# Performance work log

Measured on AMD Instinct MI355X. Metric: run time of the kernel, lower is better.

Reference implementation:

```python
import jax, jax.numpy as jnp
import numpy as np

B, C_IN, N, WIDTH, MODES, OUT_CH, DEG = 4, 3, 8192, 128, 32, 1, 16
NT = B * N


def _gelu(v):
    return jax.nn.gelu(v, approximate=False)  # torch nn.GELU default = exact erf


def _seg_mean(msg, dst, n):
    # PyG aggr='mean': zero-degree nodes get 0
    s = jax.ops.segment_sum(msg, dst, num_segments=n)
    c = jax.ops.segment_sum(jnp.ones((dst.shape[0], 1), msg.dtype), dst, num_segments=n)
    return s / jnp.maximum(c, 1.0)


def _inorm(v, eps=1e-5):
    # nn.InstanceNorm1d(width): per (batch, channel) over length, no affine
    m = v.mean(-1, keepdims=True)
    var = v.var(-1, keepdims=True)
    return (v - m) / jnp.sqrt(var + eps)


def _fourier(v, wr, wi):
    n = v.shape[-1]
    vf = jnp.fft.rfft(v, axis=-1)  # [B, width, n//2+1] complex64
    w = wr + 1j * wi               # [width, width, modes]
    of = jnp.einsum('bix,iox->box', vf[:, :, :MODES], w)
    of = jnp.pad(of, ((0, 0), (0, 0), (0, n // 2 + 1 - MODES)))
    return jnp.fft.irfft(of, n=n, axis=-1)


def _conv1(v, w, b):
    # Conv1d kernel_size=1 == channel-mixing GEMM
    return jnp.einsum('bin,oi->bon', v, w) + b[None, :, None]


def setup_inputs() -> dict:
    key = jax.random.key(0)
    ks = jax.random.split(key, 24)
    x = jax.random.normal(ks[0], (B, C_IN, N), jnp.float32)
    # edges: per-graph random neighbors + self loops (radius_graph(loop=True) surrogate)
    dst = jnp.repeat(jnp.arange(NT), DEG)
    gid = dst // N
    src = jax.random.randint(ks[1], (NT * DEG,), 0, N) + gid * N
    loops = jnp.arange(NT)
    edge_index = jnp.stack([jnp.concatenate([src, loops]),
                            jnp.concatenate([dst, loops])]).astype(jnp.int32)
    s = 0.02
    scale = 1.0 / (WIDTH + WIDTH)
    inp = {
        'x': x,
        'edge_index': edge_index,
        'enc_e_w': s * jax.random.normal(ks[2], (WIDTH, 2 * C_IN), jnp.float32),
        'enc_e_b': s * jax.random.normal(ks[3], (WIDTH,), jnp.float32),
        'enc_c_w': s * jax.random.normal(ks[4], (WIDTH, WIDTH), jnp.float32),
        'enc_c_b': s * jax.random.normal(ks[5], (WIDTH,), jnp.float32),
        'wr': scale * jax.random.uniform(ks[6], (4, WIDTH, WIDTH, MODES), jnp.float32),
        'wi': scale * jax.random.uniform(ks[7], (4, WIDTH, WIDTH, MODES), jnp.float32),
        'w_w': s * jax.random.normal(ks[8], (4, WIDTH, WIDTH), jnp.float32),
        'w_b': s * jax.random.normal(ks[9], (4, WIDTH), jnp.float32),
        'f1_w': s * jax.random.normal(ks[10], (4, WIDTH, WIDTH), jnp.float32),
        'f1_b': s * jax.random.normal(ks[11], (4, WIDTH), jnp.float32),
        'f2_w': s * jax.random.normal(ks[12], (4, WIDTH, WIDTH), jnp.float32),
        'f2_b': s * jax.random.normal(ks[13], (4, WIDTH), jnp.float32),
        'dec1_w': s * jax.random.normal(ks[14], (2 * WIDTH, WIDTH), jnp.float32),
        'dec1_b': s * jax.random.normal(ks[15], (2 * WIDTH,), jnp.float32),
        'dec3_w': s * jax.random.normal(ks[16], (OUT_CH, 2 * WIDTH), jnp.float32),
        'dec3_b': s * jax.random.normal(ks[17], (OUT_CH,), jnp.float32),
    }
    return inp


def reference(x, edge_index, enc_e_w, enc_e_b, enc_c_w, enc_c_b, wr, wi,
              w_w, w_b, f1_w, f1_b, f2_w, f2_b, dec1_w, dec1_b, dec3_w, dec3_b):
    src, dst = edge_index[0], edge_index[1]
    xf = x.transpose(0, 2, 1).reshape(NT, C_IN)  # [B*N, C]
    # --- GNO encoder: EdgeConv -> GELU -> Collection ---
    xi, xj = xf[dst], xf[src]
    m = jnp.concatenate([xi, xj - xi], axis=1) @ enc_e_w.T + enc_e_b
    h = _gelu(_seg_mean(m, dst, NT))
    hl = h @ enc_c_w.T + enc_c_b  # linear-then-gather (CollectionLayer order)
    h = _seg_mean(hl[src], dst, NT)
    h = h.reshape(B, N, WIDTH).transpose(0, 2, 1)  # [B, width, N]
    # --- 4 FNO blocks ---
    for i in range(4):
        x1 = _inorm(_fourier(_inorm(h), wr[i], wi[i]))
        x1 = _conv1(_gelu(_conv1(x1, f1_w[i], f1_b[i])), f2_w[i], f2_b[i])
        x2 = _conv1(h, w_w[i], w_b[i])
        h = _gelu(x1 + x2)
    # --- GNO decoder: Collection -> GELU -> Collection ---
    hf = h.transpose(0, 2, 1).reshape(NT, WIDTH)
    hl = hf @ dec1_w.T + dec1_b
    h = _gelu(_seg_mean(hl[src], dst, NT))
    hl = h @ dec3_w.T + dec3_b
    h = _seg_mean(hl[src], dst, NT)
    return h.reshape(B, N, OUT_CH).transpose(0, 2, 1)  # [B, out_ch, N]
```

## Files before the change

kernel.cpp:

```cpp
#include <hip/hip_runtime.h>
#include <math.h>

#define BB    4
#define CIN   3
#define NN    8192
#define NTOT  32768
#define WD    128
#define MODES 32
#define DEG   16
#define NEDGE 17
#define TWOPI 6.28318530717958647692f

typedef _Float16 f16;
typedef _Float16 f16x8 __attribute__((ext_vector_type(8)));
typedef _Float16 f16x4 __attribute__((ext_vector_type(4)));
typedef _Float16 f16x2 __attribute__((ext_vector_type(2)));
typedef float    f32x4 __attribute__((ext_vector_type(4)));

__device__ __forceinline__ float gelu_f(float v) {
    return 0.5f * v * (1.0f + erff(v * 0.7071067811865476f));
}

__device__ __forceinline__ int swz1024(int bid) {
    int xcd = bid & 7;
    int g = xcd >> 1;
    int local = ((bid >> 3) << 1) | (xcd & 1);
    return (g << 8) | local;
}


__global__ __launch_bounds__(256) void k_tables(f16* __restrict__ nkbf,
                                                f16* __restrict__ tknh) {
    int idx = blockIdx.x * 256 + threadIdx.x;
    if (idx >= NN * MODES) return;
    int n = idx >> 5;
    int k = idx & 31;
    int m = (n * k) & (NN - 1);
    float ang = (float)m * (TWOPI / (float)NN);
    float s, c;
    sincosf(ang, &s, &c);
    if (k >= 1) {
        nkbf[n * 64 + 2 * k - 2] = (f16)c;
        nkbf[n * 64 + 2 * k - 1] = (f16)s;
        tknh[(2 * k) * NN + n]     = (f16)c;
        tknh[(2 * k + 1) * NN + n] = (f16)s;
    } else {
        nkbf[n * 64 + 62] = (f16)0.f;
        nkbf[n * 64 + 63] = (f16)0.f;
        tknh[n]      = (f16)1.f;
        tknh[NN + n] = (f16)0.f;
    }
}

__global__ __launch_bounds__(256) void k_casts(const float* __restrict__ f2w,
        const float* __restrict__ ww, const float* __restrict__ dec1w,
        const float* __restrict__ ecw, f16* __restrict__ wcat,
        f16* __restrict__ w1h, f16* __restrict__ ecwh) {
    int idx = blockIdx.x * 256 + threadIdx.x;
    if (idx < 131072) {
        int lay = idx >> 15, rem = idx & 32767;
        int o = rem >> 8, k = rem & 255;
        float v = (k < 128) ? f2w[(lay * WD + o) * WD + k]
                            : ww[(lay * WD + o) * WD + (k - 128)];
        wcat[idx] = (f16)v;
    } else if (idx < 163840) {
        int i2 = idx - 131072;
        w1h[i2] = (f16)dec1w[i2];
    } else if (idx < 180224) {
        int i3 = idx - 163840;
        ecwh[i3] = (f16)ecw[i3];
    }
}

__global__ __launch_bounds__(256) void k_twr(const float* __restrict__ wr,
        const float* __restrict__ wi, float* __restrict__ wrT, float* __restrict__ wiT) {
    const float* src = blockIdx.y ? wi : wr;
    float*       dst = blockIdx.y ? wiT : wrT;
    int ib = blockIdx.x >> 7, i = blockIdx.x & 127;
    __shared__ float tile[128][33];
    const float* s = src + ((ib * WD + i) * WD) * MODES;
    for (int e = threadIdx.x; e < WD * MODES; e += 256) {
        int o = e >> 5, k = e & 31;
        tile[o][k] = s[e];
    }
    __syncthreads();
    float* d = dst + ib * (MODES * WD * WD) + i * WD;
    for (int e = threadIdx.x; e < WD * MODES; e += 256) {
        int k = e >> 7, o = e & 127;
        d[k * WD * WD + o] = tile[o][k];
    }
}


__global__ __launch_bounds__(256) void k_enc_fused(const float* __restrict__ x,
        const int* __restrict__ src, const float* __restrict__ ew,
        const float* __restrict__ eb, f16* __restrict__ h1) {
    int tid = threadIdx.x;
    int t0 = blockIdx.x * 64;
    int b = t0 >> 13;
    const float* xg0 = x + (size_t)(b * 3 + 0) * NN;
    const float* xg1 = x + (size_t)(b * 3 + 1) * NN;
    const float* xg2 = x + (size_t)(b * 3 + 2) * NN;
    __shared__ float agg[64][8];
    {
        int nl = tid >> 2;
        int sub = tid & 3;
        int t = t0 + nl;
        int4 sl = *(const int4*)&src[t * DEG + sub * 4];
        int i0 = sl.x & (NN - 1), i1 = sl.y & (NN - 1);
        int i2 = sl.z & (NN - 1), i3 = sl.w & (NN - 1);
        float a0 = xg0[i0] + xg0[i1] + xg0[i2] + xg0[i3];
        float a1 = xg1[i0] + xg1[i1] + xg1[i2] + xg1[i3];
        float a2 = xg2[i0] + xg2[i1] + xg2[i2] + xg2[i3];
        a0 += __shfl_xor(a0, 1); a0 += __shfl_xor(a0, 2);
        a1 += __shfl_xor(a1, 1); a1 += __shfl_xor(a1, 2);
        a2 += __shfl_xor(a2, 1); a2 += __shfl_xor(a2, 2);
        if (sub == 0) {
            int n_ = t & (NN - 1);
            float xi0 = xg0[n_], xi1 = xg1[n_], xi2 = xg2[n_];
            agg[nl][0] = xi0; agg[nl][1] = xi1; agg[nl][2] = xi2;
            agg[nl][3] = (a0 + xi0) * (1.f / NEDGE) - xi0;
            agg[nl][4] = (a1 + xi1) * (1.f / NEDGE) - xi1;
            agg[nl][5] = (a2 + xi2) * (1.f / NEDGE) - xi2;
        }
    }
    __syncthreads();
    int o = tid & 127, half = tid >> 7;
    const float* w = ew + o * 6;
    float w0 = w[0], w1 = w[1], w2 = w[2], w3 = w[3], w4 = w[4], w5 = w[5];
    float bb = eb[o];
    #pragma unroll 4
    for (int g = 0; g < 32; ++g) {
        int n2 = half * 32 + g;
        float acc = bb + w0 * agg[n2][0] + w1 * agg[n2][1] + w2 * agg[n2][2]
                       + w3 * agg[n2][3] + w4 * agg[n2][4] + w5 * agg[n2][5];
        h1[(size_t)(t0 + n2) * WD + o] = (f16)gelu_f(acc);
    }
}

__device__ __forceinline__ void gather4_to_lds(const f16* __restrict__ hin,
        const int* __restrict__ src, int t0, int tid, f16* At) {
    int wv = tid >> 6;
    int lane = tid & 63;
    int nd = lane >> 4;
    int cl = lane & 15;
    #pragma unroll
    for (int it = 0; it < 2; ++it) {
        int nl = wv * 8 + it * 4 + nd;
        int t = t0 + nl;
        f16x8 v = *(const f16x8*)&hin[(size_t)t * WD + cl * 8];
        float a0 = (float)v[0], a1 = (float)v[1], a2 = (float)v[2], a3 = (float)v[3];
        float a4 = (float)v[4], a5 = (float)v[5], a6 = (float)v[6], a7 = (float)v[7];
        const int* sl = src + t * DEG;
        #pragma unroll
        for (int d = 0; d < DEG; ++d) {
            int nb = sl[d];
            f16x8 u = *(const f16x8*)&hin[(size_t)nb * WD + cl * 8];
            a0 += (float)u[0]; a1 += (float)u[1]; a2 += (float)u[2]; a3 += (float)u[3];
            a4 += (float)u[4]; a5 += (float)u[5]; a6 += (float)u[6]; a7 += (float)u[7];
        }
        const float sc = 1.f / NEDGE;
        f16x8 r;
        r[0] = (f16)(a0 * sc); r[1] = (f16)(a1 * sc); r[2] = (f16)(a2 * sc); r[3] = (f16)(a3 * sc);
        r[4] = (f16)(a4 * sc); r[5] = (f16)(a5 * sc); r[6] = (f16)(a6 * sc); r[7] = (f16)(a7 * sc);
        *(f16x8*)&At[nl * 136 + cl * 8] = r;
    }
}

__global__ __launch_bounds__(256, 4) void k_gather_lin_mfma(
        const f16* __restrict__ hin, const int* __restrict__ src,
        const f16* __restrict__ ecwh, const float* __restrict__ bias,
        f16* __restrict__ outp) {
    int tid = threadIdx.x;
    int ebid = swz1024(blockIdx.x);
    int t0 = ebid * 32;
    int b = ebid >> 8;
    int n0 = (ebid & 255) * 32;
    __shared__ f16 At[32 * 136];
    gather4_to_lds(hin, src, t0, tid, At);
    __syncthreads();
    int w = tid >> 6, l = tid & 63, lg = l >> 4, ln = l & 15;
    f32x4 acc[2][2] = {};
    #pragma unroll
    for (int kc = 0; kc < 4; ++kc) {
        f16x8 wa[2], ab[2];
        #pragma unroll
        for (int i = 0; i < 2; ++i)
            wa[i] = *(const f16x8*)&ecwh[((2 * w + i) * 16 + ln) * WD + kc * 32 + lg * 8];
        #pragma unroll
        for (int j = 0; j < 2; ++j)
            ab[j] = *(const f16x8*)&At[(j * 16 + ln) * 136 + kc * 32 + lg * 8];
        #pragma unroll
        for (int i = 0; i < 2; ++i)
            #pragma unroll
            for (int j = 0; j < 2; ++j)
                acc[i][j] = __builtin_amdgcn_mfma_f32_16x16x32_f16(wa[i], ab[j], acc[i][j], 0, 0, 0);
    }
    #pragma unroll
    for (int i = 0; i < 2; ++i) {
        int cb = (2 * w + i) * 16 + lg * 4;
        float b0 = bias[cb], b1 = bias[cb + 1], b2 = bias[cb + 2], b3 = bias[cb + 3];
        #pragma unroll
        for (int j = 0; j < 2; ++j) {
            int n_ = n0 + j * 16 + ln;
            outp[(size_t)(b * WD + cb + 0) * NN + n_] = (f16)(acc[i][j][0] + b0);
            outp[(size_t)(b * WD + cb + 1) * NN + n_] = (f16)(acc[i][j][1] + b1);
            outp[(size_t)(b * WD + cb + 2) * NN + n_] = (f16)(acc[i][j][2] + b2);
            outp[(size_t)(b * WD + cb + 3) * NN + n_] = (f16)(acc[i][j][3] + b3);
        }
    }
}


__global__ __launch_bounds__(256, 2) void k_dft_mfma(const f16* __restrict__ h,
        const f16* __restrict__ tknh, float* __restrict__ part) {
    int bid = blockIdx.x;
    int sp = bid >> 3;
    int r0 = (bid & 7) * 64;
    int wv = threadIdx.x >> 6, l = threadIdx.x & 63, lg = l >> 4, ln = l & 15;
    int row = r0 + wv * 16;
    f32x4 acc[4] = {};
    const f16* ha = h + (size_t)(row + ln) * NN + sp * 256 + lg * 8;
    const f16* tb = tknh + (size_t)ln * NN + sp * 256 + lg * 8;
    #pragma unroll
    for (int st = 0; st < 8; ++st) {
        f16x8 a = *(const f16x8*)&ha[st * 32];
        #pragma unroll
        for (int tj = 0; tj < 4; ++tj) {
            f16x8 b = *(const f16x8*)&tb[(size_t)(tj * 16) * NN + st * 32];
            acc[tj] = __builtin_amdgcn_mfma_f32_16x16x32_f16(a, b, acc[tj], 0, 0, 0);
        }
    }
    float* pr = part + ((size_t)sp * 512 + row) * 64;
    #pragma unroll
    for (int tj = 0; tj < 4; ++tj)
        #pragma unroll
        for (int q = 0; q < 4; ++q)
            pr[(lg * 4 + q) * 64 + tj * 16 + ln] = acc[tj][q];
}

__global__ __launch_bounds__(256) void k_dft_fin3(const f16* __restrict__ h,
        const float* __restrict__ part, float* __restrict__ vf) {
    int row = blockIdx.x * 4 + (threadIdx.x >> 6);
    int lane = threadIdx.x & 63;
    const f16* hr = h + (size_t)row * NN;
    float s = 0.f, q = 0.f;
    #pragma unroll
    for (int i = 0; i < 16; ++i) {
        f16x8 v = *(const f16x8*)&hr[lane * 8 + i * 512];
        #pragma unroll
        for (int j = 0; j < 8; ++j) {
            float f = (float)v[j];
            s += f; q += f * f;
        }
    }
    #pragma unroll
    for (int off = 32; off; off >>= 1) {
        s += __shfl_xor(s, off);
        q += __shfl_xor(q, off);
    }
    float mu  = s * (1.f / NN);
    float var = q * (1.f / NN) - mu * mu;
    float s1  = 1.f / sqrtf(fmaxf(var, 0.f) + 1e-5f);
    float D = 0.f;
    #pragma unroll
    for (int p = 0; p < 32; ++p)
        D += part[(size_t)(p * 512 + row) * 64 + lane];
    float v;
    if (lane < 2) v = 0.f;
    else          v = (lane & 1) ? -D * s1 : D * s1;
    vf[row * 64 + lane] = v;
}

__global__ __launch_bounds__(128) void k_spec(const float* __restrict__ vf,
        const float* __restrict__ wrT, const float* __restrict__ wiT,
        float* __restrict__ of, int lay) {
    int b = blockIdx.x / 31;
    int k = blockIdx.x - b * 31 + 1;
    int o = threadIdx.x;
    __shared__ float vr[WD], vi[WD];
    vr[o] = vf[(b * WD + o) * 64 + 2 * k];
    vi[o] = vf[(b * WD + o) * 64 + 2 * k + 1];
    __syncthreads();
    const float* wrk = wrT + ((size_t)(lay * MODES + k) * WD) * WD + o;
    const float* wik = wiT + ((size_t)(lay * MODES + k) * WD) * WD + o;
    float ore = 0.f, oim = 0.f;
    for (int i = 0; i < WD; ++i) {
        float a = vr[i], bq = vi[i];
        float w0 = wrk[i * WD], w1 = wik[i * WD];
        ore += a * w0 - bq * w1;
        oim += a * w1 + bq * w0;
    }
    of[(b * WD + o) * 64 + 2 * k]     = ore;
    of[(b * WD + o) * 64 + 2 * k + 1] = oim;
}

__global__ __launch_bounds__(256) void k_coef(const float* __restrict__ of,
        const float* __restrict__ f1w, f16* __restrict__ GB) {
    int b = blockIdx.x >> 3;
    int c0 = (blockIdx.x & 7) * 16;
    __shared__ float ofl[WD][66];
    __shared__ float fw[16][WD];
    __shared__ float scl[WD];
    for (int e = threadIdx.x; e < WD * 64; e += 256) {
        int o = e >> 6, kc = e & 63;
        ofl[o][kc] = of[(b * WD + o) * 64 + kc];
    }
    for (int e = threadIdx.x; e < 16 * WD; e += 256) {
        int cl = e >> 7, i = e & 127;
        fw[cl][i] = f1w[(c0 + cl) * WD + i];
    }
    __syncthreads();
    if (threadIdx.x < WD) {
        int o = threadIdx.x;
        float s = 0.f;
        for (int kc = 2; kc < 64; ++kc) { float v = ofl[o][kc]; s += v * v; }
        float var = s * (2.f / ((float)NN * (float)NN));
        scl[o] = (2.f / (float)NN) / sqrtf(var + 1e-5f);
    }
    __syncthreads();
    for (int e = threadIdx.x; e < 16 * 62; e += 256) {
        int cl = e / 62, kc = e - cl * 62 + 2;
        float a = 0.f;
        for (int o = 0; o < WD; ++o)
            a += fw[cl][o] * (ofl[o][kc] * scl[o]);
        if (kc & 1) a = -a;
        GB[(b * WD + c0 + cl) * 64 + (kc - 2)] = (f16)a;
    }
    if (threadIdx.x < 32) {
        int cl = threadIdx.x >> 1;
        GB[(b * WD + c0 + cl) * 64 + 62 + (threadIdx.x & 1)] = (f16)0.f;
    }
}

__global__ __launch_bounds__(256, 2) void k_fno(const f16* __restrict__ hc,
        const f16* __restrict__ GB, const f16* __restrict__ nkbf,
        const f16* __restrict__ wcat, const float* __restrict__ f1b,
        const float* __restrict__ f2b, const float* __restrict__ wb,
        f16* __restrict__ hn) {
    int tid = threadIdx.x;
    int b = blockIdx.x >> 7;
    int n0 = (blockIdx.x & 127) * 64;
    int w = tid >> 6, l = tid & 63, lg = l >> 4, ln = l & 15;
    __shared__ f16 tS[64 * 136];
    __shared__ f16 hS[64 * 136];
    f16x8 hreg[4];
    #pragma unroll
    for (int p = 0; p < 4; ++p) {
        int idx = p * 256 + tid;
        int c = idx >> 3, n8 = idx & 7;
        hreg[p] = *(const f16x8*)&hc[(size_t)(b * WD + c) * NN + n0 + n8 * 8];
    }
    f32x4 acc1[2][4] = {};
    #pragma unroll
    for (int kc = 0; kc < 2; ++kc) {
        f16x8 ga[2], tb[4];
        #pragma unroll
        for (int i = 0; i < 2; ++i)
            ga[i] = *(const f16x8*)&GB[(size_t)(b * WD + (2 * w + i) * 16 + ln) * 64 + kc * 32 + lg * 8];
        #pragma unroll
        for (int j = 0; j < 4; ++j)
            tb[j] = *(const f16x8*)&nkbf[(size_t)(n0 + j * 16 + ln) * 64 + kc * 32 + lg * 8];
        #pragma unroll
        for (int i = 0; i < 2; ++i)
            #pragma unroll
            for (int j = 0; j < 4; ++j)
                acc1[i][j] = __builtin_amdgcn_mfma_f32_16x16x32_f16(ga[i], tb[j], acc1[i][j], 0, 0, 0);
    }
    #pragma unroll
    for (int i = 0; i < 2; ++i) {
        int cb = (2 * w + i) * 16 + lg * 4;
        float b0 = f1b[cb], b1 = f1b[cb + 1], b2 = f1b[cb + 2], b3 = f1b[cb + 3];
        #pragma unroll
        for (int j = 0; j < 4; ++j) {
            int n_ = j * 16 + ln;
            f16x4 o4;
            o4[0] = (f16)gelu_f(acc1[i][j][0] + b0);
            o4[1] = (f16)gelu_f(acc1[i][j][1] + b1);
            o4[2] = (f16)gelu_f(acc1[i][j][2] + b2);
            o4[3] = (f16)gelu_f(acc1[i][j][3] + b3);
            *(f16x4*)&tS[n_ * 136 + cb] = o4;
        }
    }
    #pragma unroll
    for (int p = 0; p < 4; ++p) {
        int idx = p * 256 + tid;
        int c = idx >> 3, n8 = idx & 7;
        #pragma unroll
        for (int q = 0; q < 8; ++q)
            hS[(n8 * 8 + q) * 136 + c] = hreg[p][q];
    }
    __syncthreads();
    f32x4 acc2[2][4] = {};
    #pragma unroll
    for (int kc = 0; kc < 8; ++kc) {
        const f16* Xs = (kc < 4) ? (tS + kc * 32) : (hS + (kc - 4) * 32);
        f16x8 wa[2], xb[4];
        #pragma unroll
        for (int i = 0; i < 2; ++i)
            wa[i] = *(const f16x8*)&wcat[(size_t)((2 * w + i) * 16 + ln) * 256 + kc * 32 + lg * 8];
        #pragma unroll
        for (int j = 0; j < 4; ++j)
            xb[j] = *(const f16x8*)&Xs[(j * 16 + ln) * 136 + lg * 8];
        #pragma unroll
        for (int i = 0; i < 2; ++i)
            #pragma unroll
            for (int j = 0; j < 4; ++j)
                acc2[i][j] = __builtin_amdgcn_mfma_f32_16x16x32_f16(wa[i], xb[j], acc2[i][j], 0, 0, 0);
    }
    #pragma unroll
    for (int i = 0; i < 2; ++i) {
        int ob = (2 * w + i) * 16 + lg * 4;
        float b0 = f2b[ob] + wb[ob];
        float b1 = f2b[ob + 1] + wb[ob + 1];
        float b2 = f2b[ob + 2] + wb[ob + 2];
        float b3 = f2b[ob + 3] + wb[ob + 3];
        #pragma unroll
        for (int j = 0; j < 4; ++j) {
            int n_ = n0 + j * 16 + ln;
            hn[(size_t)(b * WD + ob + 0) * NN + n_] = (f16)gelu_f(acc2[i][j][0] + b0);
            hn[(size_t)(b * WD + ob + 1) * NN + n_] = (f16)gelu_f(acc2[i][j][1] + b1);
            hn[(size_t)(b * WD + ob + 2) * NN + n_] = (f16)gelu_f(acc2[i][j][2] + b2);
            hn[(size_t)(b * WD + ob + 3) * NN + n_] = (f16)gelu_f(acc2[i][j][3] + b3);
        }
    }
}


__global__ __launch_bounds__(256) void k_tr_hf(const f16* __restrict__ h,
        f16* __restrict__ hf) {
    int bx = blockIdx.x;
    int b = bx >> 10;
    int ct = (bx >> 8) & 3;
    int nt = bx & 255;
    __shared__ f16 tile[32][34];
    int tx = threadIdx.x & 31, ty = threadIdx.x >> 5;
    int c0 = ct * 32, n0 = nt * 32;
    #pragma unroll
    for (int j = 0; j < 32; j += 8)
        tile[ty + j][tx] = h[(size_t)(b * WD + c0 + ty + j) * NN + n0 + tx];
    __syncthreads();
    #pragma unroll
    for (int j = 0; j < 32; j += 8)
        hf[(size_t)(b * NN + n0 + ty + j) * WD + c0 + tx] = tile[tx][ty + j];
}

__global__ __launch_bounds__(256, 4) void k_dec_mfma(const f16* __restrict__ hf,
        const int* __restrict__ src, const f16* __restrict__ w1h,
        const float* __restrict__ b1, const float* __restrict__ w3,
        const float* __restrict__ b3, float* __restrict__ z) {
    int tid = threadIdx.x;
    int t0 = swz1024(blockIdx.x) * 32;
    __shared__ f16 At[32 * 136];
    __shared__ float zl[16 * 32];
    gather4_to_lds(hf, src, t0, tid, At);
    __syncthreads();
    int w = tid >> 6, l = tid & 63, lg = l >> 4, ln = l & 15;
    f32x4 acc[4][2] = {};
    #pragma unroll
    for (int kc = 0; kc < 4; ++kc) {
        f16x8 wa[4], ab[2];
        #pragma unroll
        for (int u = 0; u < 4; ++u)
            wa[u] = *(const f16x8*)&w1h[(size_t)((w * 4 + u) * 16 + ln) * WD + kc * 32 + lg * 8];
        #pragma unroll
        for (int j = 0; j < 2; ++j)
            ab[j] = *(const f16x8*)&At[(j * 16 + ln) * 136 + kc * 32 + lg * 8];
        #pragma unroll
        for (int u = 0; u < 4; ++u)
            #pragma unroll
            for (int j = 0; j < 2; ++j)
                acc[u][j] = __builtin_amdgcn_mfma_f32_16x16x32_f16(wa[u], ab[j], acc[u][j], 0, 0, 0);
    }
    float pz[2] = {0.f, 0.f};
    #pragma unroll
    for (int u = 0; u < 4; ++u) {
        int jb = (w * 4 + u) * 16 + lg * 4;
        float b1r0 = b1[jb], b1r1 = b1[jb + 1], b1r2 = b1[jb + 2], b1r3 = b1[jb + 3];
        float w3r0 = w3[jb], w3r1 = w3[jb + 1], w3r2 = w3[jb + 2], w3r3 = w3[jb + 3];
        #pragma unroll
        for (int j = 0; j < 2; ++j) {
            pz[j] += w3r0 * gelu_f(acc[u][j][0] + b1r0);
            pz[j] += w3r1 * gelu_f(acc[u][j][1] + b1r1);
            pz[j] += w3r2 * gelu_f(acc[u][j][2] + b1r2);
            pz[j] += w3r3 * gelu_f(acc[u][j][3] + b1r3);
        }
    }
    #pragma unroll
    for (int j = 0; j < 2; ++j)
        zl[(w * 4 + lg) * 32 + j * 16 + ln] = pz[j];
    __syncthreads();
    if (tid < 32) {
        float s = b3[0];
        #pragma unroll
        for (int g = 0; g < 16; ++g) s += zl[g * 32 + tid];
        z[t0 + tid] = s;
    }
}

__global__ __launch_bounds__(256) void k_out(const float* __restrict__ z,
        const int* __restrict__ src, float* __restrict__ outp) {
    int t = blockIdx.x * 256 + threadIdx.x;
    if (t >= NTOT) return;
    const int* sl = src + t * DEG;
    float acc = z[t];
    #pragma unroll
    for (int d = 0; d < DEG; ++d) acc += z[sl[d]];
    outp[t] = acc * (1.f / NEDGE);
}


extern "C" void kernel_launch(void* const* d_in, const int* in_sizes, int n_in,
                              void* d_out, int out_size, void* d_ws, size_t ws_size,
                              hipStream_t stream) {
    const float* x       = (const float*)d_in[0];
    const int*   ei      = (const int*)  d_in[1];
    const float* enc_e_w = (const float*)d_in[2];
    const float* enc_e_b = (const float*)d_in[3];
    const float* enc_c_w = (const float*)d_in[4];
    const float* enc_c_b = (const float*)d_in[5];
    const float* wr      = (const float*)d_in[6];
    const float* wi      = (const float*)d_in[7];
    const float* w_w     = (const float*)d_in[8];
    const float* w_b     = (const float*)d_in[9];
    const float* f1_w    = (const float*)d_in[10];
    const float* f1_b    = (const float*)d_in[11];
    const float* f2_w    = (const float*)d_in[12];
    const float* f2_b    = (const float*)d_in[13];
    const float* dec1_w  = (const float*)d_in[14];
    const float* dec1_b  = (const float*)d_in[15];
    const float* dec3_w  = (const float*)d_in[16];
    const float* dec3_b  = (const float*)d_in[17];
    float* outp = (float*)d_out;
    float* ws = (float*)d_ws;

    float* wrT   = ws;
    float* wiT   = wrT + 2097152;
    float* part  = wiT + 2097152;
    float* zb    = part + 1048576;
    float* vf    = zb + 32768;
    float* of    = vf + 32768;
    f16* h1h  = (f16*)(of + 32768);
    f16* H0   = h1h + 4194304;
    f16* H1   = H0 + 4194304;
    f16* nkbf = H1 + 4194304;
    f16* tknh = nkbf + 524288;
    f16* wcatB= tknh + 524288;
    f16* w1h  = wcatB + 131072;
    f16* ecwh = w1h + 32768;
    f16* GB   = ecwh + 16384;
    f16* hfh  = h1h;

    k_tables<<<1024, 256, 0, stream>>>(nkbf, tknh);
    k_casts<<<704, 256, 0, stream>>>(f2_w, w_w, dec1_w, enc_c_w, wcatB, w1h, ecwh);
    k_twr<<<dim3(512, 2), 256, 0, stream>>>(wr, wi, wrT, wiT);

    k_enc_fused<<<512, 256, 0, stream>>>(x, ei, enc_e_w, enc_e_b, h1h);
    k_gather_lin_mfma<<<1024, 256, 0, stream>>>(h1h, ei, ecwh, enc_c_b, H0);

    for (int lay = 0; lay < 4; ++lay) {
        f16* hc = (lay & 1) ? H1 : H0;
        f16* hn = (lay & 1) ? H0 : H1;
        k_dft_mfma<<<256, 256, 0, stream>>>(hc, tknh, part);
        k_dft_fin3<<<128, 256, 0, stream>>>(hc, part, vf);
        k_spec<<<124, 128, 0, stream>>>(vf, wrT, wiT, of, lay);
        k_coef<<<32, 256, 0, stream>>>(of, f1_w + lay * WD * WD, GB);
        k_fno<<<512, 256, 0, stream>>>(hc, GB, nkbf, wcatB + lay * WD * 256,
                                       f1_b + lay * WD, f2_b + lay * WD,
                                       w_b + lay * WD, hn);
    }

    k_tr_hf<<<4096, 256, 0, stream>>>(H0, hfh);
    k_dec_mfma<<<1024, 256, 0, stream>>>(hfh, ei, w1h, dec1_b, dec3_w, dec3_b, zb);
    k_out<<<128, 256, 0, stream>>>(zb, ei, outp);
}
```

Baseline: 252.3 us.

## Merge setup kernels, fuse DFT finalize into spectral kernel, halve FNO tiles

Three setup kernels become one launch with block-range dispatch. The DFT kernel now splits the mode columns across waves, doubling the grid, and accumulates per-row sum of squares as it goes. A new k_specfin reads the partial sums to get mean and variance (mode 0 gives the sum) and does the spectral mixing with 256 threads splitting the input channels. This removes k_dft_fin3's second full read of h and one launch per layer. k_fno tiles shrink from 64 to 32 positions with launch bounds raised to 4, doubling the grid for occupancy at the cost of more redundant weight loads per output.

```diff
diff --git a/kernel.cpp b/kernel.cpp
--- a/kernel.cpp
+++ b/kernel.cpp
@@ -29,65 +29,65 @@
 }
 
 
-__global__ __launch_bounds__(256) void k_tables(f16* __restrict__ nkbf,
-                                                f16* __restrict__ tknh) {
-    int idx = blockIdx.x * 256 + threadIdx.x;
-    if (idx >= NN * MODES) return;
-    int n = idx >> 5;
-    int k = idx & 31;
-    int m = (n * k) & (NN - 1);
-    float ang = (float)m * (TWOPI / (float)NN);
-    float s, c;
-    sincosf(ang, &s, &c);
-    if (k >= 1) {
-        nkbf[n * 64 + 2 * k - 2] = (f16)c;
-        nkbf[n * 64 + 2 * k - 1] = (f16)s;
-        tknh[(2 * k) * NN + n]     = (f16)c;
-        tknh[(2 * k + 1) * NN + n] = (f16)s;
+__global__ __launch_bounds__(256) void k_setup(const float* __restrict__ f2w,
+        const float* __restrict__ ww, const float* __restrict__ dec1w,
+        const float* __restrict__ ecw, const float* __restrict__ wr,
+        const float* __restrict__ wi, f16* __restrict__ nkbf,
+        f16* __restrict__ tknh, f16* __restrict__ wcat, f16* __restrict__ w1h,
+        f16* __restrict__ ecwh, float* __restrict__ wrT, float* __restrict__ wiT) {
+    int bid = blockIdx.x;
+    if (bid < 1024) {
+        int idx = bid * 256 + threadIdx.x;
+        int n = idx >> 5;
+        int k = idx & 31;
+        int m = (n * k) & (NN - 1);
+        float ang = (float)m * (TWOPI / (float)NN);
+        float s, c;
+        sincosf(ang, &s, &c);
+        if (k >= 1) {
+            nkbf[n * 64 + 2 * k - 2] = (f16)c;
+            nkbf[n * 64 + 2 * k - 1] = (f16)s;
+            tknh[(2 * k) * NN + n]     = (f16)c;
+            tknh[(2 * k + 1) * NN + n] = (f16)s;
+        } else {
+            nkbf[n * 64 + 62] = (f16)0.f;
+            nkbf[n * 64 + 63] = (f16)0.f;
+            tknh[n]      = (f16)1.f;
+            tknh[NN + n] = (f16)0.f;
+        }
+    } else if (bid < 1728) {
+        int idx = (bid - 1024) * 256 + threadIdx.x;
+        if (idx < 131072) {
+            int lay = idx >> 15, rem = idx & 32767;
+            int o = rem >> 8, k = rem & 255;
+            float v = (k < 128) ? f2w[(lay * WD + o) * WD + k]
+                                : ww[(lay * WD + o) * WD + (k - 128)];
+            wcat[idx] = (f16)v;
+        } else if (idx < 163840) {
+            int i2 = idx - 131072;
+            w1h[i2] = (f16)dec1w[i2];
+        } else if (idx < 180224) {
+            int i3 = idx - 163840;
+            ecwh[i3] = (f16)ecw[i3];
+        }
     } else {
-        nkbf[n * 64 + 62] = (f16)0.f;
-        nkbf[n * 64 + 63] = (f16)0.f;
-        tknh[n]      = (f16)1.f;
-        tknh[NN + n] = (f16)0.f;
-    }
-}
-
-__global__ __launch_bounds__(256) void k_casts(const float* __restrict__ f2w,
-        const float* __restrict__ ww, const float* __restrict__ dec1w,
-        const float* __restrict__ ecw, f16* __restrict__ wcat,
-        f16* __restrict__ w1h, f16* __restrict__ ecwh) {
-    int idx = blockIdx.x * 256 + threadIdx.x;
-    if (idx < 131072) {
-        int lay = idx >> 15, rem = idx & 32767;
-        int o = rem >> 8, k = rem & 255;
-        float v = (k < 128) ? f2w[(lay * WD + o) * WD + k]
-                            : ww[(lay * WD + o) * WD + (k - 128)];
-        wcat[idx] = (f16)v;
-    } else if (idx < 163840) {
-        int i2 = idx - 131072;
-        w1h[i2] = (f16)dec1w[i2];
-    } else if (idx < 180224) {
-        int i3 = idx - 163840;
-        ecwh[i3] = (f16)ecw[i3];
-    }
-}
-
-__global__ __launch_bounds__(256) void k_twr(const float* __restrict__ wr,
-        const float* __restrict__ wi, float* __restrict__ wrT, float* __restrict__ wiT) {
-    const float* src = blockIdx.y ? wi : wr;
-    float*       dst = blockIdx.y ? wiT : wrT;
-    int ib = blockIdx.x >> 7, i = blockIdx.x & 127;
-    __shared__ float tile[128][33];
-    const float* s = src + ((ib * WD + i) * WD) * MODES;
-    for (int e = threadIdx.x; e < WD * MODES; e += 256) {
-        int o = e >> 5, k = e & 31;
-        tile[o][k] = s[e];
-    }
-    __syncthreads();
-    float* d = dst + ib * (MODES * WD * WD) + i * WD;
-    for (int e = threadIdx.x; e < WD * MODES; e += 256) {
-        int k = e >> 7, o = e & 127;
-        d[k * WD * WD + o] = tile[o][k];
+        int twb = bid - 1728;
+        const float* src = (twb >> 9) ? wi : wr;
+        float*       dst = (twb >> 9) ? wiT : wrT;
+        int xx = twb & 511;
+        int ib = xx >> 7, i = xx & 127;
+        __shared__ float tile[128][33];
+        const float* s = src + ((size_t)(ib * WD + i) * WD) * MODES;
+        for (int e = threadIdx.x; e < WD * MODES; e += 256) {
+            int o = e >> 5, k = e & 31;
+            tile[o][k] = s[e];
+        }
+        __syncthreads();
+        float* d = dst + (size_t)ib * (MODES * WD * WD) + i * WD;
+        for (int e = threadIdx.x; e < WD * MODES; e += 256) {
+            int k = e >> 7, o = e & 127;
+            d[(size_t)k * WD * WD + o] = tile[o][k];
+        }
     }
 }
 
@@ -213,86 +213,93 @@
 
 
 __global__ __launch_bounds__(256, 2) void k_dft_mfma(const f16* __restrict__ h,
-        const f16* __restrict__ tknh, float* __restrict__ part) {
+        const f16* __restrict__ tknh, float* __restrict__ part,
+        float* __restrict__ sqp) {
     int bid = blockIdx.x;
-    int sp = bid >> 3;
-    int r0 = (bid & 7) * 64;
+    int sp = bid >> 4;
+    int r0 = (bid & 15) * 32;
     int wv = threadIdx.x >> 6, l = threadIdx.x & 63, lg = l >> 4, ln = l & 15;
-    int row = r0 + wv * 16;
-    f32x4 acc[4] = {};
+    int rh = wv & 1, kh = wv >> 1;
+    int row = r0 + rh * 16;
+    f32x4 acc[2] = {};
     const f16* ha = h + (size_t)(row + ln) * NN + sp * 256 + lg * 8;
-    const f16* tb = tknh + (size_t)ln * NN + sp * 256 + lg * 8;
+    const f16* tb = tknh + (size_t)(kh * 32 + ln) * NN + sp * 256 + lg * 8;
+    float sq = 0.f;
     #pragma unroll
     for (int st = 0; st < 8; ++st) {
         f16x8 a = *(const f16x8*)&ha[st * 32];
-        #pragma unroll
-        for (int tj = 0; tj < 4; ++tj) {
+        if (kh == 0) {
+            #pragma unroll
+            for (int j = 0; j < 8; ++j) { float f = (float)a[j]; sq += f * f; }
+        }
+        #pragma unroll
+        for (int tj = 0; tj < 2; ++tj) {
             f16x8 b = *(const f16x8*)&tb[(size_t)(tj * 16) * NN + st * 32];
             acc[tj] = __builtin_amdgcn_mfma_f32_16x16x32_f16(a, b, acc[tj], 0, 0, 0);
         }
     }
     float* pr = part + ((size_t)sp * 512 + row) * 64;
     #pragma unroll
-    for (int tj = 0; tj < 4; ++tj)
+    for (int tj = 0; tj < 2; ++tj)
         #pragma unroll
         for (int q = 0; q < 4; ++q)
-            pr[(lg * 4 + q) * 64 + tj * 16 + ln] = acc[tj][q];
-}
-
-__global__ __launch_bounds__(256) void k_dft_fin3(const f16* __restrict__ h,
-        const float* __restrict__ part, float* __restrict__ vf) {
-    int row = blockIdx.x * 4 + (threadIdx.x >> 6);
-    int lane = threadIdx.x & 63;
-    const f16* hr = h + (size_t)row * NN;
-    float s = 0.f, q = 0.f;
-    #pragma unroll
-    for (int i = 0; i < 16; ++i) {
-        f16x8 v = *(const f16x8*)&hr[lane * 8 + i * 512];
-        #pragma unroll
-        for (int j = 0; j < 8; ++j) {
-            float f = (float)v[j];
-            s += f; q += f * f;
-        }
-    }
-    #pragma unroll
-    for (int off = 32; off; off >>= 1) {
-        s += __shfl_xor(s, off);
-        q += __shfl_xor(q, off);
-    }
-    float mu  = s * (1.f / NN);
-    float var = q * (1.f / NN) - mu * mu;
-    float s1  = 1.f / sqrtf(fmaxf(var, 0.f) + 1e-5f);
-    float D = 0.f;
-    #pragma unroll
-    for (int p = 0; p < 32; ++p)
-        D += part[(size_t)(p * 512 + row) * 64 + lane];
-    float v;
-    if (lane < 2) v = 0.f;
-    else          v = (lane & 1) ? -D * s1 : D * s1;
-    vf[row * 64 + lane] = v;
-}
-
-__global__ __launch_bounds__(128) void k_spec(const float* __restrict__ vf,
-        const float* __restrict__ wrT, const float* __restrict__ wiT,
-        float* __restrict__ of, int lay) {
+            pr[(lg * 4 + q) * 64 + (kh * 2 + tj) * 16 + ln] = acc[tj][q];
+    if (kh == 0) {
+        sq += __shfl_xor(sq, 16);
+        sq += __shfl_xor(sq, 32);
+        if (lg == 0) sqp[sp * 512 + row + ln] = sq;
+    }
+}
+
+__global__ __launch_bounds__(256) void k_specfin(const float* __restrict__ part,
+        const float* __restrict__ sqp, const float* __restrict__ wrT,
+        const float* __restrict__ wiT, float* __restrict__ of, int lay) {
     int b = blockIdx.x / 31;
     int k = blockIdx.x - b * 31 + 1;
-    int o = threadIdx.x;
-    __shared__ float vr[WD], vi[WD];
-    vr[o] = vf[(b * WD + o) * 64 + 2 * k];
-    vi[o] = vf[(b * WD + o) * 64 + 2 * k + 1];
-    __syncthreads();
+    int tid = threadIdx.x;
+    __shared__ float vr[WD], vi[WD], s1s[WD];
+    __shared__ float ofp[2][2][WD];
+    if (tid < 128) {
+        int row = b * 128 + tid;
+        float D0 = 0.f, sq = 0.f;
+        for (int p = 0; p < 32; ++p) {
+            D0 += part[((size_t)p * 512 + row) * 64];
+            sq += sqp[p * 512 + row];
+        }
+        float mu  = D0 * (1.f / NN);
+        float var = sq * (1.f / NN) - mu * mu;
+        s1s[tid] = 1.f / sqrtf(fmaxf(var, 0.f) + 1e-5f);
+    }
+    __syncthreads();
+    {
+        int i = tid & 127;
+        int half = tid >> 7;
+        int row = b * 128 + i;
+        int kc = 2 * k + half;
+        float D = 0.f;
+        for (int p = 0; p < 32; ++p)
+            D += part[((size_t)p * 512 + row) * 64 + kc];
+        float v = D * s1s[i];
+        if (half) vi[i] = -v; else vr[i] = v;
+    }
+    __syncthreads();
+    int o = tid & 127, ih = tid >> 7;
     const float* wrk = wrT + ((size_t)(lay * MODES + k) * WD) * WD + o;
     const float* wik = wiT + ((size_t)(lay * MODES + k) * WD) * WD + o;
     float ore = 0.f, oim = 0.f;
-    for (int i = 0; i < WD; ++i) {
+    for (int i = ih * 64; i < ih * 64 + 64; ++i) {
         float a = vr[i], bq = vi[i];
         float w0 = wrk[i * WD], w1 = wik[i * WD];
         ore += a * w0 - bq * w1;
         oim += a * w1 + bq * w0;
     }
-    of[(b * WD + o) * 64 + 2 * k]     = ore;
-    of[(b * WD + o) * 64 + 2 * k + 1] = oim;
+    ofp[ih][0][o] = ore;
+    ofp[ih][1][o] = oim;
+    __syncthreads();
+    if (tid < 128) {
+        of[(b * WD + tid) * 64 + 2 * k]     = ofp[0][0][tid] + ofp[1][0][tid];
+        of[(b * WD + tid) * 64 + 2 * k + 1] = ofp[0][1][tid] + ofp[1][1][tid];
+    }
 }
 
 __global__ __launch_bounds__(256) void k_coef(const float* __restrict__ of,
@@ -333,38 +340,38 @@
     }
 }
 
-__global__ __launch_bounds__(256, 2) void k_fno(const f16* __restrict__ hc,
+__global__ __launch_bounds__(256, 4) void k_fno(const f16* __restrict__ hc,
         const f16* __restrict__ GB, const f16* __restrict__ nkbf,
         const f16* __restrict__ wcat, const float* __restrict__ f1b,
         const float* __restrict__ f2b, const float* __restrict__ wb,
         f16* __restrict__ hn) {
     int tid = threadIdx.x;
-    int b = blockIdx.x >> 7;
-    int n0 = (blockIdx.x & 127) * 64;
+    int b = blockIdx.x >> 8;
+    int n0 = (blockIdx.x & 255) * 32;
     int w = tid >> 6, l = tid & 63, lg = l >> 4, ln = l & 15;
-    __shared__ f16 tS[64 * 136];
-    __shared__ f16 hS[64 * 136];
-    f16x8 hreg[4];
-    #pragma unroll
-    for (int p = 0; p < 4; ++p) {
+    __shared__ f16 tS[32 * 136];
+    __shared__ f16 hS[32 * 136];
+    f16x8 hreg[2];
+    #pragma unroll
+    for (int p = 0; p < 2; ++p) {
         int idx = p * 256 + tid;
-        int c = idx >> 3, n8 = idx & 7;
+        int c = idx >> 2, n8 = idx & 3;
         hreg[p] = *(const f16x8*)&hc[(size_t)(b * WD + c) * NN + n0 + n8 * 8];
     }
-    f32x4 acc1[2][4] = {};
+    f32x4 acc1[2][2] = {};
     #pragma unroll
     for (int kc = 0; kc < 2; ++kc) {
-        f16x8 ga[2], tb[4];
+        f16x8 ga[2], tb[2];
         #pragma unroll
         for (int i = 0; i < 2; ++i)
             ga[i] = *(const f16x8*)&GB[(size_t)(b * WD + (2 * w + i) * 16 + ln) * 64 + kc * 32 + lg * 8];
         #pragma unroll
-        for (int j = 0; j < 4; ++j)
+        for (int j = 0; j < 2; ++j)
             tb[j] = *(const f16x8*)&nkbf[(size_t)(n0 + j * 16 + ln) * 64 + kc * 32 + lg * 8];
         #pragma unroll
         for (int i = 0; i < 2; ++i)
             #pragma unroll
-            for (int j = 0; j < 4; ++j)
+            for (int j = 0; j < 2; ++j)
                 acc1[i][j] = __builtin_amdgcn_mfma_f32_16x16x32_f16(ga[i], tb[j], acc1[i][j], 0, 0, 0);
     }
     #pragma unroll
@@ -372,7 +379,7 @@
         int cb = (2 * w + i) * 16 + lg * 4;
         float b0 = f1b[cb], b1 = f1b[cb + 1], b2 = f1b[cb + 2], b3 = f1b[cb + 3];
         #pragma unroll
-        for (int j = 0; j < 4; ++j) {
+        for (int j = 0; j < 2; ++j) {
             int n_ = j * 16 + ln;
             f16x4 o4;
             o4[0] = (f16)gelu_f(acc1[i][j][0] + b0);
@@ -383,29 +390,29 @@
         }
     }
     #pragma unroll
-    for (int p = 0; p < 4; ++p) {
+    for (int p = 0; p < 2; ++p) {
         int idx = p * 256 + tid;
-        int c = idx >> 3, n8 = idx & 7;
+        int c = idx >> 2, n8 = idx & 3;
         #pragma unroll
         for (int q = 0; q < 8; ++q)
             hS[(n8 * 8 + q) * 136 + c] = hreg[p][q];
     }
     __syncthreads();
-    f32x4 acc2[2][4] = {};
+    f32x4 acc2[2][2] = {};
     #pragma unroll
     for (int kc = 0; kc < 8; ++kc) {
         const f16* Xs = (kc < 4) ? (tS + kc * 32) : (hS + (kc - 4) * 32);
-        f16x8 wa[2], xb[4];
+        f16x8 wa[2], xb[2];
         #pragma unroll
         for (int i = 0; i < 2; ++i)
             wa[i] = *(const f16x8*)&wcat[(size_t)((2 * w + i) * 16 + ln) * 256 + kc * 32 + lg * 8];
         #pragma unroll
-        for (int j = 0; j < 4; ++j)
+        for (int j = 0; j < 2; ++j)
             xb[j] = *(const f16x8*)&Xs[(j * 16 + ln) * 136 + lg * 8];
         #pragma unroll
         for (int i = 0; i < 2; ++i)
             #pragma unroll
-            for (int j = 0; j < 4; ++j)
+            for (int j = 0; j < 2; ++j)
                 acc2[i][j] = __builtin_amdgcn_mfma_f32_16x16x32_f16(wa[i], xb[j], acc2[i][j], 0, 0, 0);
     }
     #pragma unroll
@@ -416,7 +423,7 @@
         float b2 = f2b[ob + 2] + wb[ob + 2];
         float b3 = f2b[ob + 3] + wb[ob + 3];
         #pragma unroll
-        for (int j = 0; j < 4; ++j) {
+        for (int j = 0; j < 2; ++j) {
             int n_ = n0 + j * 16 + ln;
             hn[(size_t)(b * WD + ob + 0) * NN + n_] = (f16)gelu_f(acc2[i][j][0] + b0);
             hn[(size_t)(b * WD + ob + 1) * NN + n_] = (f16)gelu_f(acc2[i][j][1] + b1);
@@ -537,9 +544,9 @@
     float* wrT   = ws;
     float* wiT   = wrT + 2097152;
     float* part  = wiT + 2097152;
-    float* zb    = part + 1048576;
-    float* vf    = zb + 32768;
-    float* of    = vf + 32768;
+    float* sqp   = part + 1048576;
+    float* zb    = sqp + 16384;
+    float* of    = zb + 32768;
     f16* h1h  = (f16*)(of + 32768);
     f16* H0   = h1h + 4194304;
     f16* H1   = H0 + 4194304;
@@ -551,9 +558,8 @@
     f16* GB   = ecwh + 16384;
     f16* hfh  = h1h;
 
-    k_tables<<<1024, 256, 0, stream>>>(nkbf, tknh);
-    k_casts<<<704, 256, 0, stream>>>(f2_w, w_w, dec1_w, enc_c_w, wcatB, w1h, ecwh);
-    k_twr<<<dim3(512, 2), 256, 0, stream>>>(wr, wi, wrT, wiT);
+    k_setup<<<2752, 256, 0, stream>>>(f2_w, w_w, dec1_w, enc_c_w, wr, wi,
+                                      nkbf, tknh, wcatB, w1h, ecwh, wrT, wiT);
 
     k_enc_fused<<<512, 256, 0, stream>>>(x, ei, enc_e_w, enc_e_b, h1h);
     k_gather_lin_mfma<<<1024, 256, 0, stream>>>(h1h, ei, ecwh, enc_c_b, H0);
@@ -561,13 +567,12 @@
     for (int lay = 0; lay < 4; ++lay) {
         f16* hc = (lay & 1) ? H1 : H0;
         f16* hn = (lay & 1) ? H0 : H1;
-        k_dft_mfma<<<256, 256, 0, stream>>>(hc, tknh, part);
-        k_dft_fin3<<<128, 256, 0, stream>>>(hc, part, vf);
-        k_spec<<<124, 128, 0, stream>>>(vf, wrT, wiT, of, lay);
+        k_dft_mfma<<<512, 256, 0, stream>>>(hc, tknh, part, sqp);
+        k_specfin<<<124, 256, 0, stream>>>(part, sqp, wrT, wiT, of, lay);
         k_coef<<<32, 256, 0, stream>>>(of, f1_w + lay * WD * WD, GB);
-        k_fno<<<512, 256, 0, stream>>>(hc, GB, nkbf, wcatB + lay * WD * 256,
-                                       f1_b + lay * WD, f2_b + lay * WD,
-                                       w_b + lay * WD, hn);
+        k_fno<<<1024, 256, 0, stream>>>(hc, GB, nkbf, wcatB + lay * WD * 256,
+                                        f1_b + lay * WD, f2_b + lay * WD,
+                                        w_b + lay * WD, hn);
     }
 
     k_tr_hf<<<4096, 256, 0, stream>>>(H0, hfh);
```

Result: slower. 279.7 us (+10.9%).
